# Kernel optimization log

Hardware: AMD Instinct MI355X
Metric: run time of the kernel (lower is better)

Reference implementation:

```python
import jax, jax.numpy as jnp
import numpy as np

# ---------- constants ----------
EPS = 1e-5
_rng = np.random.default_rng(0)
_P = _rng.normal(size=(8, 3))
_P /= np.linalg.norm(_P, axis=1, keepdims=True)

def _y2_np(p):
    x, y, z = p[:, 0], p[:, 1], p[:, 2]
    return np.stack([x * y, y * z, 3 * z * z - 1, x * z, x * x - y * y], axis=-1)

_A2 = np.linalg.pinv(_y2_np(_P)).astype(np.float32)  # [5,8]
P_C = jnp.asarray(_P.astype(np.float32))
A2_C = jnp.asarray(_A2)
NORM_CONST = np.float32(1.0 / np.sqrt(20.0))  # avg_num_neighbors ** -0.5
# res update (buffer zeros, not learnable): sigmoid(0)=0.5
_U = 0.5
C_OLD = np.float32(1.0 / np.sqrt(_U * _U + 1.0))
C_NEW = np.float32(_U * C_OLD)


def _y2(p):  # real l=2 monomial basis on unit vectors
    x, y, z = p[..., 0], p[..., 1], p[..., 2]
    return jnp.stack([x * y, y * z, 3.0 * z * z - 1.0, x * z, x * x - y * y], axis=-1)


def _frame(v):  # [E,3] -> R [E,3,3] with R @ v_hat = z
    n = v / jnp.linalg.norm(v, axis=-1, keepdims=True)
    z = jnp.array([0.0, 0.0, 1.0], v.dtype)
    xa = jnp.array([1.0, 0.0, 0.0], v.dtype)
    a = jnp.where(jnp.abs(n[:, 2:3]) < 0.99, z, xa)
    e1 = jnp.cross(a, n)
    e1 = e1 / jnp.linalg.norm(e1, axis=-1, keepdims=True)
    e2 = jnp.cross(n, e1)
    return jnp.stack([e1, e2, n], axis=1)


def _wigner_d2(R):  # [E,3,3] -> D2 [E,5,5] via sample-point fit
    pts = jnp.einsum('pj,eij->epi', P_C, R)  # R @ p_k, [E,8,3]
    M = _y2(pts)  # [E,8,5] = Y_P @ D^T
    Dt = jnp.einsum('ap,epb->eab', A2_C, M)  # [E,5,5]
    return jnp.swapaxes(Dt, 1, 2)


def _sln(x, w0, b0, w1, w2):  # separable equivariant layernorm, 32x0e+16x1e+8x2e
    s = x[:, :32]
    v1 = x[:, 32:80].reshape(-1, 16, 3)
    v2 = x[:, 80:120].reshape(-1, 8, 5)
    mu = jnp.mean(s, axis=-1, keepdims=True)
    var = jnp.mean((s - mu) ** 2, axis=-1, keepdims=True)
    s = (s - mu) * jax.lax.rsqrt(var + EPS) * w0 + b0
    var1 = jnp.mean(v1 ** 2, axis=(1, 2))  # degree-balanced component variance
    var2 = jnp.mean(v2 ** 2, axis=(1, 2))
    inv = jax.lax.rsqrt(0.5 * (var1 + var2) + EPS)[:, None, None]
    v1 = v1 * inv * w1[None, :, None]
    v2 = v2 * inv * w2[None, :, None]
    return jnp.concatenate([s, v1.reshape(-1, 48), v2.reshape(-1, 40)], axis=-1)


def _ir_linear(x, W0, b0, W1, W2):  # irreps-wise linear 32x0e+16x1e+8x2e -> same
    s = x[:, :32] @ (W0 / np.sqrt(32.0)) + b0
    v1 = jnp.einsum('eui,uv->evi', x[:, 32:80].reshape(-1, 16, 3), W1) / np.sqrt(16.0)
    v2 = jnp.einsum('eui,uv->evi', x[:, 80:120].reshape(-1, 8, 5), W2) / np.sqrt(8.0)
    return jnp.concatenate([s, v1.reshape(-1, 48), v2.reshape(-1, 40)], axis=-1)


def _so2(x_cat, R, D2f, D2b, w):  # SO2 linear with per-edge dynamic weights
    E = x_cat.shape[0]
    w0 = w[:, :8960].reshape(E, 112, 80)
    w1r = w[:, 8960:10112].reshape(E, 48, 24)
    w1i = w[:, 10112:11264].reshape(E, 48, 24)
    w2r = w[:, 11264:11392].reshape(E, 16, 8)
    w2i = w[:, 11392:11520].reshape(E, 16, 8)
    # split concatenated [in + hidden] blocks
    s = jnp.concatenate([x_cat[:, :32], x_cat[:, 120:152]], axis=-1)  # [E,64]
    v1 = jnp.concatenate([x_cat[:, 32:80].reshape(E, 16, 3),
                          x_cat[:, 152:200].reshape(E, 16, 3)], axis=1)  # [E,32,3]
    v2 = jnp.concatenate([x_cat[:, 80:120].reshape(E, 8, 5),
                          x_cat[:, 200:240].reshape(E, 16 // 2, 5)], axis=1)  # [E,16,5]
    # rotate into edge-aligned frame
    v1 = jnp.einsum('eij,euj->eui', R, v1)
    v2 = jnp.einsum('eij,euj->eui', D2f, v2)
    in0 = jnp.concatenate([s, v1[:, :, 1], v2[:, :, 2]], axis=-1)   # m=0, [E,112]
    inn1 = jnp.concatenate([v1[:, :, 0], v2[:, :, 1]], axis=-1)     # m=-1, [E,48]
    inp1 = jnp.concatenate([v1[:, :, 2], v2[:, :, 3]], axis=-1)     # m=+1
    inn2 = v2[:, :, 0]  # m=-2
    inp2 = v2[:, :, 4]  # m=+2
    out0 = jnp.einsum('ei,eio->eo', in0, w0) / np.sqrt(112.0)
    op1 = (jnp.einsum('ei,eio->eo', inp1, w1r) - jnp.einsum('ei,eio->eo', inn1, w1i)) / np.sqrt(48.0)
    on1 = (jnp.einsum('ei,eio->eo', inn1, w1r) + jnp.einsum('ei,eio->eo', inp1, w1i)) / np.sqrt(48.0)
    op2 = (jnp.einsum('ei,eio->eo', inp2, w2r) - jnp.einsum('ei,eio->eo', inn2, w2i)) / np.sqrt(16.0)
    on2 = (jnp.einsum('ei,eio->eo', inn2, w2r) + jnp.einsum('ei,eio->eo', inp2, w2i)) / np.sqrt(16.0)
    s_out = out0[:, :56]
    y1 = jnp.stack([on1[:, :16], out0[:, 56:72], op1[:, :16]], axis=-1)  # [E,16,3]
    y2o = jnp.stack([on2, on1[:, 16:24], out0[:, 72:80], op1[:, 16:24], op2], axis=-1)  # [E,8,5]
    # rotate back
    y1 = jnp.einsum('eij,euj->eui', jnp.swapaxes(R, 1, 2), y1)
    y2o = jnp.einsum('eij,euj->eui', D2b, y2o)
    return jnp.concatenate([s_out, y1.reshape(E, 48), y2o.reshape(E, 40)], axis=-1)  # [E,144]


def _gate(m):  # 32x0e scalars | 24x0e gates | 16x1e+8x2e gated
    s = jax.nn.silu(m[:, :32])
    g = jax.nn.sigmoid(m[:, 32:56])
    v1 = m[:, 56:104].reshape(-1, 16, 3) * g[:, :16, None]
    v2 = m[:, 104:144].reshape(-1, 8, 5) * g[:, 16:24, None]
    return jnp.concatenate([s, v1.reshape(-1, 48), v2.reshape(-1, 40)], axis=-1)


def _env(m, we):  # E3ElementLinear: per-mul elementwise weights
    s = m[:, :32] * we[:, :32]
    v1 = m[:, 32:80].reshape(-1, 16, 3) * we[:, 32:48, None]
    v2 = m[:, 80:120].reshape(-1, 8, 5) * we[:, 48:56, None]
    return jnp.concatenate([s, v1.reshape(-1, 48), v2.reshape(-1, 40)], axis=-1)


def setup_inputs() -> dict:
    key = jax.random.key(0)
    ks = jax.random.split(key, 16)
    N, E, L = 512, 10240, 128
    inp = {
        'latents': jax.random.normal(ks[0], (E, L), jnp.float32),
        'node_features': jax.random.normal(ks[1], (N, 120), jnp.float32),
        'hidden_features': jax.random.normal(ks[2], (E, 120), jnp.float32),
        'node_onehot': jnp.ones((N, 16), jnp.float32),
        'edge_vector': jax.random.normal(ks[3], (E, 3), jnp.float32),
        'W_tp': jax.random.normal(ks[4], (L, 11520), jnp.float32),
        'W_env': jax.random.normal(ks[5], (L, 56), jnp.float32),
        'sln_w0': jnp.ones((32,), jnp.float32),
        'sln_b0': jnp.zeros((32,), jnp.float32),
        'sln_w1': jnp.ones((16,), jnp.float32),
        'sln_w2': jnp.ones((8,), jnp.float32),
        'Wp0': jax.random.normal(ks[6], (32, 32), jnp.float32),
        'bp0': jnp.zeros((32,), jnp.float32),
        'Wp1': jax.random.normal(ks[7], (16, 16), jnp.float32),
        'Wp2': jax.random.normal(ks[8], (8, 8), jnp.float32),
        'Wr0': jax.random.normal(ks[9], (32, 32), jnp.float32),
        'br0': jnp.zeros((32,), jnp.float32),
        'Wr1': jax.random.normal(ks[10], (16, 16), jnp.float32),
        'Wr2': jax.random.normal(ks[11], (8, 8), jnp.float32),
        'atom_type': jax.random.randint(ks[12], (N,), 0, 10, jnp.int32),
        'edge_index': jax.random.randint(ks[13], (2, E), 0, N, jnp.int32),
        'active_edges': jnp.arange(E, dtype=jnp.int32),
    }
    return inp


def reference(latents, node_features, hidden_features, node_onehot, edge_vector,
              W_tp, W_env, sln_w0, sln_b0, sln_w1, sln_w2,
              Wp0, bp0, Wp1, Wp2, Wr0, br0, Wr1, Wr2,
              atom_type, edge_index, active_edges):
    n_nodes = node_features.shape[0]
    center = edge_index[0][active_edges]
    nf = _sln(node_features, sln_w0, sln_b0, sln_w1, sln_w2)
    x_cat = jnp.concatenate([nf[center], hidden_features], axis=-1)  # [E,240]
    v = edge_vector[active_edges]
    R = _frame(v)
    D2f = _wigner_d2(R)
    D2b = _wigner_d2(jnp.swapaxes(R, 1, 2))
    wdyn = latents @ (W_tp / np.sqrt(128.0))  # per-edge dynamic SO2 weights
    msg = _so2(x_cat, R, D2f, D2b, wdyn)
    msg = _gate(msg)
    msg = _ir_linear(msg, Wp0, bp0, Wp1, Wp2)
    wenv = latents[active_edges] @ (W_env / np.sqrt(128.0))
    weighted = _env(msg, wenv)
    new_nf = jax.ops.segment_sum(weighted, center, num_segments=n_nodes)
    new_nf = new_nf * NORM_CONST
    res = _ir_linear(node_features, Wr0, br0, Wr1, Wr2)
    return C_NEW * new_nf + C_OLD * res
```

## Files before the change

### kernel.cpp

```cpp
#include <hip/hip_runtime.h>
#include <math.h>

#define E_TOT   10240
#define N_NODES 512
#define NCOL    11520

typedef unsigned short ushort_t;
typedef unsigned int   uint_t;
typedef __bf16 bf16x8 __attribute__((ext_vector_type(8)));
typedef float  f32x4  __attribute__((ext_vector_type(4)));

constexpr float EPSF        = 1e-5f;
constexpr float INV_SQRT128 = 0.08838834764831845f;
constexpr float INV_SQRT112 = 0.09449111825230681f;
constexpr float INV_SQRT48  = 0.14433756729740643f;
constexpr float INV_SQRT32  = 0.17677669529663687f;
constexpr float INV_SQRT16  = 0.25f;
constexpr float INV_SQRT8   = 0.35355339059327373f;
constexpr float SC0 = INV_SQRT128 * INV_SQRT112;
constexpr float SC1 = INV_SQRT128 * INV_SQRT48;
constexpr float SC2 = INV_SQRT128 * INV_SQRT16;
constexpr float C_OLD_ = 0.8944271909999159f;
constexpr float C_NEW_ = 0.4472135954999579f;
constexpr float NORMC  = 0.22360679774997896f;

__device__ __forceinline__ float wsum(float v) {
#pragma unroll
  for (int off = 32; off > 0; off >>= 1) v += __shfl_xor(v, off, 64);
  return v;
}

__device__ __forceinline__ ushort_t f2bf(float x) {
  uint_t u = __float_as_uint(x);
  u = (u + 0x7fffu + ((u >> 16) & 1u)) >> 16;
  return (ushort_t)u;
}

__device__ __forceinline__ void wigner5(const float q[9], float D[25]) {
  const float q0x=q[0],q0y=q[1],q0z=q[2];
  const float q1x=q[3],q1y=q[4],q1z=q[5];
  const float q2x=q[6],q2y=q[7],q2z=q[8];
  D[0]  = q0x*q1y + q1x*q0y;
  D[1]  = q0y*q1z + q1y*q0z;
  D[2]  = 0.5f*(q0z*q1z);
  D[3]  = q0x*q1z + q1x*q0z;
  D[4]  = 0.5f*(q0x*q1x - q0y*q1y);
  D[5]  = q1x*q2y + q2x*q1y;
  D[6]  = q1y*q2z + q2y*q1z;
  D[7]  = 0.5f*(q1z*q2z);
  D[8]  = q1x*q2z + q2x*q1z;
  D[9]  = 0.5f*(q1x*q2x - q1y*q2y);
  D[10] = 6.f*q2x*q2y;
  D[11] = 6.f*q2y*q2z;
  D[12] = 0.5f*(3.f*q2z*q2z - 1.f);
  D[13] = 6.f*q2x*q2z;
  D[14] = 1.5f*(q2x*q2x - q2y*q2y);
  D[15] = q0x*q2y + q2x*q0y;
  D[16] = q0y*q2z + q2y*q0z;
  D[17] = 0.5f*(q0z*q2z);
  D[18] = q0x*q2z + q2x*q0z;
  D[19] = 0.5f*(q0x*q2x - q0y*q2y);
  D[20] = 2.f*(q0x*q0y - q1x*q1y);
  D[21] = 2.f*(q0y*q0z - q1y*q1z);
  D[22] = 0.5f*(q0z*q0z - q1z*q1z);
  D[23] = 2.f*(q0x*q0z - q1x*q1z);
  D[24] = 0.5f*((q0x*q0x - q1x*q1x) - (q0y*q0y - q1y*q1y));
}

__global__ void k0_latpack(const float* __restrict__ lat,
                           ushort_t* __restrict__ lath, ushort_t* __restrict__ latl) {
  int idx = blockIdx.x*256 + threadIdx.x;
  if (idx >= E_TOT*128) return;
  float x = lat[idx];
  ushort_t h = f2bf(x);
  float hf = __uint_as_float(((uint_t)h) << 16);
  lath[idx] = h;
  latl[idx] = f2bf(x - hf);
}

__global__ void k_pack(const float* __restrict__ Wtp, ushort_t* __restrict__ Wp) {
  const int nt = blockIdx.x;
  const int t = threadIdx.x;
  const int kc = t >> 6, lane = t & 63;
  const int m = lane & 15, kg = lane >> 4;
  int j, mt;
  if (nt < 560)      { j = nt/7; mt = nt - j*7; }
  else if (nt < 704) { int r = nt-560; int p = r/3; j = 80+p; mt = r - p*3; }
  else               { j = 128 + (nt-704); mt = 0; }
  const int i = mt*16 + m;
  int c; float sc;
  if (j < 80)       { c = i*80 + j;               sc = SC0; }
  else if (j < 104) { c = 8960  + i*24 + (j-80);  sc = SC1; }
  else if (j < 128) { c = 10112 + i*24 + (j-104); sc = SC1; }
  else if (j < 136) { c = 11264 + i*8  + (j-128); sc = SC2; }
  else              { c = 11392 + i*8  + (j-136); sc = SC2; }
  ushort_t hi[8], lo[8];
#pragma unroll
  for (int jj = 0; jj < 8; ++jj) {
    int l = kc*32 + kg*8 + jj;
    float w = Wtp[(size_t)l*NCOL + c] * sc;
    ushort_t h = f2bf(w);
    float hf = __uint_as_float(((uint_t)h) << 16);
    hi[jj] = h;
    lo[jj] = f2bf(w - hf);
  }
  size_t base = ((size_t)nt*8 + kc*2)*512 + (size_t)lane*8;
#pragma unroll
  for (int jj = 0; jj < 8; ++jj) {
    Wp[base + jj]       = hi[jj];
    Wp[base + 512 + jj] = lo[jj];
  }
}

__global__ void k1_sln(const float* __restrict__ x_all,
                       const float* __restrict__ w0, const float* __restrict__ b0,
                       const float* __restrict__ w1, const float* __restrict__ w2,
                       float* __restrict__ nf) {
  const int n = blockIdx.x;
  const int t = threadIdx.x;
  const float* x = x_all + n*120;
  float xs = (t < 32) ? x[t] : 0.f;
  float ssum = wsum(xs);
  float ssq  = wsum(xs*xs);
  float mu   = ssum * (1.f/32.f);
  float var  = ssq * (1.f/32.f) - mu*mu;
  float istd = rsqrtf(var + EPSF);
  float q1 = (t < 48) ? x[32+t] : 0.f;
  float v1s = wsum(q1*q1);
  float q2 = (t < 40) ? x[80+t] : 0.f;
  float v2s = wsum(q2*q2);
  float inv = rsqrtf(0.5f*(v1s*(1.f/48.f) + v2s*(1.f/40.f)) + EPSF);
  for (int j = t; j < 120; j += 64) {
    float val = x[j], r;
    if (j < 32)      r = (val - mu)*istd*w0[j] + b0[j];
    else if (j < 80) r = val*inv*w1[(j-32)/3];
    else             r = val*inv*w2[(j-80)/5];
    nf[n*120 + j] = r;
  }
}

__global__ void k2_edge_prep(const float* __restrict__ hid,
                             const float* __restrict__ evec,
                             const int*   __restrict__ eidx,
                             const int*   __restrict__ act,
                             const float* __restrict__ nf,
                             float* __restrict__ invec,
                             float* __restrict__ Rm,
                             float* __restrict__ D2bm) {
  const int e = blockIdx.x*blockDim.x + threadIdx.x;
  if (e >= E_TOT) return;
  const int ae  = act[e];
  const int ctr = eidx[ae];
  float vx = evec[ae*3+0], vy = evec[ae*3+1], vz = evec[ae*3+2];
  float rn = rsqrtf(vx*vx + vy*vy + vz*vz);
  float nx = vx*rn, ny = vy*rn, nz = vz*rn;
  float e1x, e1y, e1z;
  if (fabsf(nz) < 0.99f) { e1x = -ny; e1y = nx;  e1z = 0.f; }
  else                   { e1x = 0.f; e1y = -nz; e1z = ny;  }
  float rl = rsqrtf(e1x*e1x + e1y*e1y + e1z*e1z);
  e1x *= rl; e1y *= rl; e1z *= rl;
  float e2x = ny*e1z - nz*e1y;
  float e2y = nz*e1x - nx*e1z;
  float e2z = nx*e1y - ny*e1x;
  float R[9] = {e1x,e1y,e1z, e2x,e2y,e2z, nx,ny,nz};
#pragma unroll
  for (int j = 0; j < 9; ++j) Rm[e*9 + j] = R[j];
  float Df[25];
  wigner5(R, Df);
  float Rt[9] = {R[0],R[3],R[6], R[1],R[4],R[7], R[2],R[5],R[8]};
  float Db[25];
  wigner5(Rt, Db);
#pragma unroll
  for (int j = 0; j < 25; ++j) D2bm[e*25 + j] = Db[j];
  const float* xa = nf  + (size_t)ctr*120;
  const float* xb = hid + (size_t)e*120;
  float* iv = invec + (size_t)e*240;
#pragma unroll
  for (int j = 0; j < 32; ++j) { iv[j] = xa[j]; iv[32+j] = xb[j]; }
#pragma unroll
  for (int u = 0; u < 32; ++u) {
    const float* src = (u < 16) ? (xa + 32 + 3*u) : (xb + 32 + 3*(u-16));
    float px = src[0], py = src[1], pz = src[2];
    float rx = R[0]*px + R[1]*py + R[2]*pz;
    float ry = R[3]*px + R[4]*py + R[5]*pz;
    float rz = R[6]*px + R[7]*py + R[8]*pz;
    iv[64+u]  = ry;
    iv[112+u] = rx;
    iv[160+u] = rz;
  }
#pragma unroll
  for (int u = 0; u < 16; ++u) {
    const float* src = (u < 8) ? (xa + 80 + 5*u) : (xb + 80 + 5*(u-8));
    float p0 = src[0], p1 = src[1], p2 = src[2], p3 = src[3], p4 = src[4];
    float d[5];
#pragma unroll
    for (int i = 0; i < 5; ++i)
      d[i] = Df[i*5+0]*p0 + Df[i*5+1]*p1 + Df[i*5+2]*p2 + Df[i*5+3]*p3 + Df[i*5+4]*p4;
    iv[96+u]  = d[2];
    iv[144+u] = d[1];
    iv[192+u] = d[3];
    iv[208+u] = d[0];
    iv[224+u] = d[4];
  }
}

__global__ void k2_wenv(const float* __restrict__ lat, const float* __restrict__ Wenv,
                        const int* __restrict__ act, float* __restrict__ wenvo) {
  const int e = blockIdx.x*4 + (threadIdx.x >> 6);
  const int o = threadIdx.x & 63;
  if (o >= 56) return;
  const int ae = act[e];
  const float* lrow = lat + (size_t)ae*128;
  float s = 0.f;
  for (int l = 0; l < 128; ++l) s += lrow[l]*Wenv[l*56 + o];
  wenvo[(size_t)e*56 + o] = s * INV_SQRT128;
}

__global__ __launch_bounds__(256, 3)
void k3_gemm(const ushort_t* __restrict__ Wp,
             const ushort_t* __restrict__ lath,
             const ushort_t* __restrict__ latl,
             const float*  __restrict__ invg,
             float* __restrict__ oa_g) {
  __shared__ float in_lds[32*244];
  const int t = threadIdx.x;
  const int eb = blockIdx.x;
  for (int i = t; i < 32*240; i += 256) {
    int e = i/240, r = i - e*240;
    in_lds[e*244 + r] = invg[(size_t)(eb*32 + e)*240 + r];
  }
  const int wave = t >> 6, lane = t & 63;
  const int le = lane & 15, g = lane >> 4;
  bf16x8 Bh[4][2], Bl[4][2];
  {
    const int e0 = eb*32 + le;
    const int ko = g*8;
#pragma unroll
    for (int kc = 0; kc < 4; ++kc) {
#pragma unroll
      for (int n = 0; n < 2; ++n) {
        size_t off = (size_t)(e0 + 16*n)*128 + kc*32 + ko;
        Bh[kc][n] = *(const bf16x8*)(lath + off);
        Bl[kc][n] = *(const bf16x8*)(latl + off);
      }
    }
  }
  __syncthreads();
  int nt = (blockIdx.y*4 + wave)*90;
  const int ntEnd = nt + 90;
  const int i0b = g*4;
  while (nt < ntEnd) {
    int j, jb, T;
    if (nt < 560)      { j = nt/7;  jb = j*7;  T = 7; }
    else if (nt < 704) { int r = nt - 560; int p = r/3; j = 80 + p; jb = 560 + p*3; T = 3; }
    else               { j = 128 + (nt - 704); jb = nt; T = 1; }
    int mt = nt - jb;
    int cnt = T - mt; { int rem = ntEnd - nt; if (cnt > rem) cnt = rem; }
    int ibA, ibB = 0, slotA, slotB = 0, two;
    float sA = 1.f;
    if (j < 80)       { two = 0; ibA = 0;   slotA = j; }
    else if (j < 104) { two = 1; int o = j-80;  ibA = 160; slotA = 80+o;            ibB = 112; slotB = 104+o; }
    else if (j < 128) { two = 1; int o = j-104; ibA = 112; slotA = 80+o; sA = -1.f; ibB = 160; slotB = 104+o; }
    else if (j < 136) { two = 1; int o = j-128; ibA = 224; slotA = 128+o;           ibB = 208; slotB = 136+o; }
    else              { two = 1; int o = j-136; ibA = 208; slotA = 128+o; sA = -1.f; ibB = 224; slotB = 136+o; }
    float aA0=0.f, aA1=0.f, aB0=0.f, aB1=0.f;
    for (int s = 0; s < cnt; ++s, ++nt, ++mt) {
      const bf16x8* ap = (const bf16x8*)Wp + (size_t)nt*512 + lane;
      f32x4 d0 = {0.f,0.f,0.f,0.f}, d1 = {0.f,0.f,0.f,0.f};
#pragma unroll
      for (int kc = 0; kc < 4; ++kc) {
        bf16x8 Ah = ap[(kc*2+0)*64];
        bf16x8 Al = ap[(kc*2+1)*64];
        d0 = __builtin_amdgcn_mfma_f32_16x16x32_bf16(Ah, Bh[kc][0], d0, 0, 0, 0);
        d1 = __builtin_amdgcn_mfma_f32_16x16x32_bf16(Ah, Bh[kc][1], d1, 0, 0, 0);
        d0 = __builtin_amdgcn_mfma_f32_16x16x32_bf16(Ah, Bl[kc][0], d0, 0, 0, 0);
        d1 = __builtin_amdgcn_mfma_f32_16x16x32_bf16(Ah, Bl[kc][1], d1, 0, 0, 0);
        d0 = __builtin_amdgcn_mfma_f32_16x16x32_bf16(Al, Bh[kc][0], d0, 0, 0, 0);
        d1 = __builtin_amdgcn_mfma_f32_16x16x32_bf16(Al, Bh[kc][1], d1, 0, 0, 0);
      }
      const int i0 = mt*16 + i0b;
      f32x4 iA0 = *(const f32x4*)&in_lds[le*244 + ibA + i0];
      f32x4 iA1 = *(const f32x4*)&in_lds[(le+16)*244 + ibA + i0];
      aA0 += d0[0]*iA0[0] + d0[1]*iA0[1] + d0[2]*iA0[2] + d0[3]*iA0[3];
      aA1 += d1[0]*iA1[0] + d1[1]*iA1[1] + d1[2]*iA1[2] + d1[3]*iA1[3];
      if (two) {
        f32x4 iB0 = *(const f32x4*)&in_lds[le*244 + ibB + i0];
        f32x4 iB1 = *(const f32x4*)&in_lds[(le+16)*244 + ibB + i0];
        aB0 += d0[0]*iB0[0] + d0[1]*iB0[1] + d0[2]*iB0[2] + d0[3]*iB0[3];
        aB1 += d1[0]*iB1[0] + d1[1]*iB1[1] + d1[2]*iB1[2] + d1[3]*iB1[3];
      }
    }
    aA0 += __shfl_xor(aA0, 16, 64); aA0 += __shfl_xor(aA0, 32, 64);
    aA1 += __shfl_xor(aA1, 16, 64); aA1 += __shfl_xor(aA1, 32, 64);
    if (two) {
      aB0 += __shfl_xor(aB0, 16, 64); aB0 += __shfl_xor(aB0, 32, 64);
      aB1 += __shfl_xor(aB1, 16, 64); aB1 += __shfl_xor(aB1, 32, 64);
    }
    if (lane < 16)      atomicAdd(&oa_g[(size_t)(eb*32 + le)*144 + slotA], sA*aA0);
    else if (lane < 32) atomicAdd(&oa_g[(size_t)(eb*32 + 16 + le)*144 + slotA], sA*aA1);
    else if (lane < 48) { if (two) atomicAdd(&oa_g[(size_t)(eb*32 + le)*144 + slotB], aB0); }
    else                { if (two) atomicAdd(&oa_g[(size_t)(eb*32 + 16 + le)*144 + slotB], aB1); }
  }
}

__global__ __launch_bounds__(256)
void k4_epi(const float* __restrict__ oa_g, const float* __restrict__ Rm,
            const float* __restrict__ D2bm, const float* __restrict__ wenvg,
            const int* __restrict__ eidx, const int* __restrict__ act,
            const float* __restrict__ Wp0, const float* __restrict__ bp0,
            const float* __restrict__ Wp1, const float* __restrict__ Wp2,
            float* __restrict__ accg) {
  __shared__ float sc[4][160];
  const int wave = threadIdx.x >> 6, lane = threadIdx.x & 63;
  const int eg = blockIdx.x*4 + wave;
  const float* o_ = oa_g + (size_t)eg*144;
  if (lane < 56) {
    float v = o_[lane];
    sc[wave][lane] = (lane < 32) ? v/(1.f + expf(-v)) : 1.f/(1.f + expf(-v));
  }
  __syncthreads();
  const float* Rr = Rm + (size_t)eg*9;
  const float* Db = D2bm + (size_t)eg*25;
  if (lane < 48) {
    int u = lane/3, cc = lane - u*3;
    float yx = o_[104+u], yy = o_[56+u], yz = o_[80+u];
    float p = Rr[cc]*yx + Rr[3+cc]*yy + Rr[6+cc]*yz;
    sc[wave][56+lane] = p * sc[wave][32+u];
  }
  if (lane >= 48 && lane < 56) {
  }
  __syncthreads();
  if (lane < 40) {
    int u = lane/5, ii = lane - u*5;
    float y0 = o_[136+u], y1v = o_[120+u], y2v = o_[72+u], y3 = o_[96+u], y4 = o_[128+u];
    float p = Db[ii*5+0]*y0 + Db[ii*5+1]*y1v + Db[ii*5+2]*y2v + Db[ii*5+3]*y3 + Db[ii*5+4]*y4;
    sc[wave][104+lane] = p * sc[wave][48+u];
  }
  __syncthreads();
  const float* we = wenvg + (size_t)eg*56;
  const int ctr = eidx[act[eg]];
  float* dst = accg + (size_t)ctr*120;
#pragma unroll
  for (int rnd = 0; rnd < 2; ++rnd) {
    int jo = rnd*64 + lane;
    if (jo < 120) {
      float val;
      if (jo < 32) {
        float s = 0.f;
#pragma unroll
        for (int i2 = 0; i2 < 32; ++i2) s += sc[wave][i2]*Wp0[i2*32 + jo];
        val = (s*INV_SQRT32 + bp0[jo]) * we[jo];
      } else if (jo < 80) {
        int jj = jo-32, v = jj/3, cc = jj - v*3;
        float s = 0.f;
#pragma unroll
        for (int u = 0; u < 16; ++u) s += sc[wave][56 + u*3 + cc]*Wp1[u*16 + v];
        val = s*INV_SQRT16*we[32+v];
      } else {
        int jj = jo-80, v = jj/5, ii = jj - v*5;
        float s = 0.f;
#pragma unroll
        for (int u = 0; u < 8; ++u) s += sc[wave][104 + u*5 + ii]*Wp2[u*8 + v];
        val = s*INV_SQRT8*we[48+v];
      }
      atomicAdd(&dst[jo], val);
    }
  }
}

__global__ void k5_final(const float* __restrict__ x_all,
                         const float* __restrict__ Wr0, const float* __restrict__ br0,
                         const float* __restrict__ Wr1, const float* __restrict__ Wr2,
                         const float* __restrict__ accg,
                         float* __restrict__ out) {
  const int n = blockIdx.x;
  const int t = threadIdx.x;
  if (t >= 120) return;
  const float* x = x_all + n*120;
  float r;
  if (t < 32) {
    float s = 0.f;
#pragma unroll
    for (int i = 0; i < 32; ++i) s += x[i]*Wr0[i*32 + t];
    r = s*INV_SQRT32 + br0[t];
  } else if (t < 80) {
    int j = t - 32, v = j/3, cp = j - 3*v;
    float s = 0.f;
#pragma unroll
    for (int u = 0; u < 16; ++u) s += x[32 + u*3 + cp]*Wr1[u*16 + v];
    r = s*INV_SQRT16;
  } else {
    int j = t - 80, v = j/5, cp = j - 5*v;
    float s = 0.f;
#pragma unroll
    for (int u = 0; u < 8; ++u) s += x[80 + u*5 + cp]*Wr2[u*8 + v];
    r = s*INV_SQRT8;
  }
  out[n*120 + t] = C_NEW_*(NORMC*accg[n*120 + t]) + C_OLD_*r;
}

extern "C" void kernel_launch(void* const* d_in, const int* in_sizes, int n_in,
                              void* d_out, int out_size, void* d_ws, size_t ws_size,
                              hipStream_t stream) {
  const float* lat  = (const float*)d_in[0];
  const float* ndf  = (const float*)d_in[1];
  const float* hid  = (const float*)d_in[2];
  const float* evec = (const float*)d_in[4];
  const float* Wtp  = (const float*)d_in[5];
  const float* Wenv = (const float*)d_in[6];
  const float* w0   = (const float*)d_in[7];
  const float* b0   = (const float*)d_in[8];
  const float* w1   = (const float*)d_in[9];
  const float* w2   = (const float*)d_in[10];
  const float* Wp0  = (const float*)d_in[11];
  const float* bp0  = (const float*)d_in[12];
  const float* Wp1  = (const float*)d_in[13];
  const float* Wp2  = (const float*)d_in[14];
  const float* Wr0  = (const float*)d_in[15];
  const float* br0  = (const float*)d_in[16];
  const float* Wr1  = (const float*)d_in[17];
  const float* Wr2  = (const float*)d_in[18];
  const int*   eidx = (const int*)d_in[20];
  const int*   act  = (const int*)d_in[21];
  float* out = (float*)d_out;

  char* p = (char*)d_ws;
  float*    nf    = (float*)(p);
  float*    invec = (float*)(p + 245760);
  float*    Rm    = (float*)(p + 10076160);
  float*    D2bm  = (float*)(p + 10444800);
  float*    wenv  = (float*)(p + 11468800);
  float*    accg  = (float*)(p + 13762560);
  float*    oa_g  = (float*)(p + 14008320);
  ushort_t* lath  = (ushort_t*)(p + 19906560);
  ushort_t* latl  = (ushort_t*)(p + 22528000);
  ushort_t* Wpack = (ushort_t*)(p + 25149440);

  hipMemsetAsync(accg, 0, 245760, stream);
  hipMemsetAsync(oa_g, 0, 5898240, stream);
  k0_latpack<<<(E_TOT*128 + 255)/256, 256, 0, stream>>>(lat, lath, latl);
  k_pack<<<720, 256, 0, stream>>>(Wtp, Wpack);
  k1_sln<<<N_NODES, 64, 0, stream>>>(ndf, w0, b0, w1, w2, nf);
  k2_edge_prep<<<E_TOT/256, 256, 0, stream>>>(hid, evec, eidx, act, nf, invec, Rm, D2bm);
  k2_wenv<<<E_TOT/4, 256, 0, stream>>>(lat, Wenv, act, wenv);
  k3_gemm<<<dim3(E_TOT/32, 2), 256, 0, stream>>>(Wpack, lath, latl, invec, oa_g);
  k4_epi<<<E_TOT/4, 256, 0, stream>>>(oa_g, Rm, D2bm, wenv, eidx, act, Wp0, bp0, Wp1, Wp2, accg);
  k5_final<<<N_NODES, 128, 0, stream>>>(ndf, Wr0, br0, Wr1, Wr2, accg, out);
}
```

Measured before the change: 336.4 us.

## Remap SO2 GEMM tiles so output channels are M and inputs are accumulated per tile

Repacks the dynamic SO2 weight tiles so each 16-row MFMA tile spans 16 output channels for one input multiplicity, rather than 16 input rows for one output. The per-tile input scalar is then broadcast from LDS and accumulated in registers, which removes the cross-lane shuffle reductions. Atomic adds happen once per segment instead of once per output column. The edge-prep kernel now writes inputs transposed (row-major by feature, edge-contiguous) so LDS staging is coalesced. The GEMM grid is doubled along y with 45 tiles per wave, and the occupancy hint rises to 4. In exchange it issues more atomics per lane at segment ends, adds templated segment code, and spreads work over more blocks.

```diff
diff --git a/kernel.cpp b/kernel.cpp
--- a/kernel.cpp
+++ b/kernel.cpp
@@ -83,17 +83,24 @@
   const int t = threadIdx.x;
   const int kc = t >> 6, lane = t & 63;
   const int m = lane & 15, kg = lane >> 4;
-  int j, mt;
-  if (nt < 560)      { j = nt/7; mt = nt - j*7; }
-  else if (nt < 704) { int r = nt-560; int p = r/3; j = 80+p; mt = r - p*3; }
-  else               { j = 128 + (nt-704); mt = 0; }
-  const int i = mt*16 + m;
+  int col, tt;
+  if (nt < 560)      { col = nt/112; tt = nt - col*112; }
+  else if (nt < 608) { col = 5;  tt = nt-560; }
+  else if (nt < 632) { col = 6;  tt = nt-608; }
+  else if (nt < 680) { col = 7;  tt = nt-632; }
+  else if (nt < 704) { col = 8;  tt = nt-680; }
+  else if (nt < 712) { col = 9;  tt = nt-704; }
+  else               { col = 10; tt = nt-712; }
   int c; float sc;
-  if (j < 80)       { c = i*80 + j;               sc = SC0; }
-  else if (j < 104) { c = 8960  + i*24 + (j-80);  sc = SC1; }
-  else if (j < 128) { c = 10112 + i*24 + (j-104); sc = SC1; }
-  else if (j < 136) { c = 11264 + i*8  + (j-128); sc = SC2; }
-  else              { c = 11392 + i*8  + (j-136); sc = SC2; }
+  switch (col) {
+    case 5:  c = 8960  + tt*24 + m;                      sc = SC1; break;
+    case 6:  c = 8960  + (2*tt + (m>>3))*24 + 16 + (m&7); sc = SC1; break;
+    case 7:  c = 10112 + tt*24 + m;                      sc = SC1; break;
+    case 8:  c = 10112 + (2*tt + (m>>3))*24 + 16 + (m&7); sc = SC1; break;
+    case 9:  c = 11264 + (2*tt + (m>>3))*8 + (m&7);      sc = SC2; break;
+    case 10: c = 11392 + (2*tt + (m>>3))*8 + (m&7);      sc = SC2; break;
+    default: c = tt*80 + col*16 + m;                     sc = SC0; break;
+  }
   ushort_t hi[8], lo[8];
 #pragma unroll
   for (int jj = 0; jj < 8; ++jj) {
@@ -144,7 +151,7 @@
                              const int*   __restrict__ eidx,
                              const int*   __restrict__ act,
                              const float* __restrict__ nf,
-                             float* __restrict__ invec,
+                             float* __restrict__ invT,
                              float* __restrict__ Rm,
                              float* __restrict__ D2bm) {
   const int e = blockIdx.x*blockDim.x + threadIdx.x;
@@ -174,9 +181,9 @@
   for (int j = 0; j < 25; ++j) D2bm[e*25 + j] = Db[j];
   const float* xa = nf  + (size_t)ctr*120;
   const float* xb = hid + (size_t)e*120;
-  float* iv = invec + (size_t)e*240;
-#pragma unroll
-  for (int j = 0; j < 32; ++j) { iv[j] = xa[j]; iv[32+j] = xb[j]; }
+#define IVST(r_, v_) invT[(size_t)(r_)*E_TOT + e] = (v_)
+#pragma unroll
+  for (int j = 0; j < 32; ++j) { IVST(j, xa[j]); IVST(32+j, xb[j]); }
 #pragma unroll
   for (int u = 0; u < 32; ++u) {
     const float* src = (u < 16) ? (xa + 32 + 3*u) : (xb + 32 + 3*(u-16));
@@ -184,9 +191,9 @@
     float rx = R[0]*px + R[1]*py + R[2]*pz;
     float ry = R[3]*px + R[4]*py + R[5]*pz;
     float rz = R[6]*px + R[7]*py + R[8]*pz;
-    iv[64+u]  = ry;
-    iv[112+u] = rx;
-    iv[160+u] = rz;
+    IVST(64+u, ry);
+    IVST(112+u, rx);
+    IVST(160+u, rz);
   }
 #pragma unroll
   for (int u = 0; u < 16; ++u) {
@@ -196,12 +203,13 @@
 #pragma unroll
     for (int i = 0; i < 5; ++i)
       d[i] = Df[i*5+0]*p0 + Df[i*5+1]*p1 + Df[i*5+2]*p2 + Df[i*5+3]*p3 + Df[i*5+4]*p4;
-    iv[96+u]  = d[2];
-    iv[144+u] = d[1];
-    iv[192+u] = d[3];
-    iv[208+u] = d[0];
-    iv[224+u] = d[4];
-  }
+    IVST(96+u,  d[2]);
+    IVST(144+u, d[1]);
+    IVST(192+u, d[3]);
+    IVST(208+u, d[0]);
+    IVST(224+u, d[4]);
+  }
+#undef IVST
 }
 
 __global__ void k2_wenv(const float* __restrict__ lat, const float* __restrict__ Wenv,
@@ -216,18 +224,68 @@
   wenvo[(size_t)e*56 + o] = s * INV_SQRT128;
 }
 
-__global__ __launch_bounds__(256, 3)
+template<bool TWO, bool PAIR>
+__device__ __forceinline__ void run_seg(
+    const bf16x8* __restrict__ W8, int f0, int f1, int tstart,
+    int multP, int multN, int slotP, int slotN, float sgnP,
+    const float* __restrict__ in_lds,
+    const bf16x8 (&Bh)[4][2], const bf16x8 (&Bl)[4][2],
+    int lane, int e0, float* __restrict__ oa) {
+  const int le = lane & 15, g = lane >> 4, gh = g >> 1;
+  f32x4 aP0 = {0,0,0,0}, aP1 = {0,0,0,0}, aN0 = {0,0,0,0}, aN1 = {0,0,0,0};
+  for (int f = f0; f < f1; ++f) {
+    const bf16x8* ap = W8 + (size_t)f*512 + lane;
+    f32x4 d0 = {0,0,0,0}, d1 = {0,0,0,0};
+#pragma unroll
+    for (int kc = 0; kc < 4; ++kc) {
+      bf16x8 Ah = ap[(kc*2+0)*64];
+      bf16x8 Al = ap[(kc*2+1)*64];
+      d0 = __builtin_amdgcn_mfma_f32_16x16x32_bf16(Ah, Bh[kc][0], d0, 0, 0, 0);
+      d1 = __builtin_amdgcn_mfma_f32_16x16x32_bf16(Ah, Bh[kc][1], d1, 0, 0, 0);
+      d0 = __builtin_amdgcn_mfma_f32_16x16x32_bf16(Ah, Bl[kc][0], d0, 0, 0, 0);
+      d1 = __builtin_amdgcn_mfma_f32_16x16x32_bf16(Ah, Bl[kc][1], d1, 0, 0, 0);
+      d0 = __builtin_amdgcn_mfma_f32_16x16x32_bf16(Al, Bh[kc][0], d0, 0, 0, 0);
+      d1 = __builtin_amdgcn_mfma_f32_16x16x32_bf16(Al, Bh[kc][1], d1, 0, 0, 0);
+    }
+    int tt = f - tstart;
+    int idx = PAIR ? (2*tt + gh) : tt;
+    float mP0 = in_lds[(multP+idx)*32 + le];
+    float mP1 = in_lds[(multP+idx)*32 + 16 + le];
+#pragma unroll
+    for (int r = 0; r < 4; ++r) { aP0[r] += mP0*d0[r]; aP1[r] += mP1*d1[r]; }
+    if (TWO) {
+      float mN0 = in_lds[(multN+idx)*32 + le];
+      float mN1 = in_lds[(multN+idx)*32 + 16 + le];
+#pragma unroll
+      for (int r = 0; r < 4; ++r) { aN0[r] += mN0*d0[r]; aN1[r] += mN1*d1[r]; }
+    }
+  }
+#pragma unroll
+  for (int r = 0; r < 4; ++r) {
+    int mm = g*4 + r;
+    int sp = slotP + (PAIR ? (mm & 7) : mm);
+    atomicAdd(&oa[(size_t)e0*144 + sp], sgnP*aP0[r]);
+    atomicAdd(&oa[(size_t)(e0+16)*144 + sp], sgnP*aP1[r]);
+    if (TWO) {
+      int sn = slotN + (PAIR ? (mm & 7) : mm);
+      atomicAdd(&oa[(size_t)e0*144 + sn], aN0[r]);
+      atomicAdd(&oa[(size_t)(e0+16)*144 + sn], aN1[r]);
+    }
+  }
+}
+
+__global__ __launch_bounds__(256, 4)
 void k3_gemm(const ushort_t* __restrict__ Wp,
              const ushort_t* __restrict__ lath,
              const ushort_t* __restrict__ latl,
-             const float*  __restrict__ invg,
+             const float*  __restrict__ invT,
              float* __restrict__ oa_g) {
-  __shared__ float in_lds[32*244];
+  __shared__ float in_lds[240*32];
   const int t = threadIdx.x;
   const int eb = blockIdx.x;
-  for (int i = t; i < 32*240; i += 256) {
-    int e = i/240, r = i - e*240;
-    in_lds[e*244 + r] = invg[(size_t)(eb*32 + e)*240 + r];
+  for (int i = t; i < 240*32; i += 256) {
+    int r = i >> 5, e = i & 31;
+    in_lds[i] = invT[(size_t)r*E_TOT + eb*32 + e];
   }
   const int wave = t >> 6, lane = t & 63;
   const int le = lane & 15, g = lane >> 4;
@@ -246,61 +304,36 @@
     }
   }
   __syncthreads();
-  int nt = (blockIdx.y*4 + wave)*90;
-  const int ntEnd = nt + 90;
-  const int i0b = g*4;
-  while (nt < ntEnd) {
-    int j, jb, T;
-    if (nt < 560)      { j = nt/7;  jb = j*7;  T = 7; }
-    else if (nt < 704) { int r = nt - 560; int p = r/3; j = 80 + p; jb = 560 + p*3; T = 3; }
-    else               { j = 128 + (nt - 704); jb = nt; T = 1; }
-    int mt = nt - jb;
-    int cnt = T - mt; { int rem = ntEnd - nt; if (cnt > rem) cnt = rem; }
-    int ibA, ibB = 0, slotA, slotB = 0, two;
-    float sA = 1.f;
-    if (j < 80)       { two = 0; ibA = 0;   slotA = j; }
-    else if (j < 104) { two = 1; int o = j-80;  ibA = 160; slotA = 80+o;            ibB = 112; slotB = 104+o; }
-    else if (j < 128) { two = 1; int o = j-104; ibA = 112; slotA = 80+o; sA = -1.f; ibB = 160; slotB = 104+o; }
-    else if (j < 136) { two = 1; int o = j-128; ibA = 224; slotA = 128+o;           ibB = 208; slotB = 136+o; }
-    else              { two = 1; int o = j-136; ibA = 208; slotA = 128+o; sA = -1.f; ibB = 224; slotB = 136+o; }
-    float aA0=0.f, aA1=0.f, aB0=0.f, aB1=0.f;
-    for (int s = 0; s < cnt; ++s, ++nt, ++mt) {
-      const bf16x8* ap = (const bf16x8*)Wp + (size_t)nt*512 + lane;
-      f32x4 d0 = {0.f,0.f,0.f,0.f}, d1 = {0.f,0.f,0.f,0.f};
-#pragma unroll
-      for (int kc = 0; kc < 4; ++kc) {
-        bf16x8 Ah = ap[(kc*2+0)*64];
-        bf16x8 Al = ap[(kc*2+1)*64];
-        d0 = __builtin_amdgcn_mfma_f32_16x16x32_bf16(Ah, Bh[kc][0], d0, 0, 0, 0);
-        d1 = __builtin_amdgcn_mfma_f32_16x16x32_bf16(Ah, Bh[kc][1], d1, 0, 0, 0);
-        d0 = __builtin_amdgcn_mfma_f32_16x16x32_bf16(Ah, Bl[kc][0], d0, 0, 0, 0);
-        d1 = __builtin_amdgcn_mfma_f32_16x16x32_bf16(Ah, Bl[kc][1], d1, 0, 0, 0);
-        d0 = __builtin_amdgcn_mfma_f32_16x16x32_bf16(Al, Bh[kc][0], d0, 0, 0, 0);
-        d1 = __builtin_amdgcn_mfma_f32_16x16x32_bf16(Al, Bh[kc][1], d1, 0, 0, 0);
-      }
-      const int i0 = mt*16 + i0b;
-      f32x4 iA0 = *(const f32x4*)&in_lds[le*244 + ibA + i0];
-      f32x4 iA1 = *(const f32x4*)&in_lds[(le+16)*244 + ibA + i0];
-      aA0 += d0[0]*iA0[0] + d0[1]*iA0[1] + d0[2]*iA0[2] + d0[3]*iA0[3];
-      aA1 += d1[0]*iA1[0] + d1[1]*iA1[1] + d1[2]*iA1[2] + d1[3]*iA1[3];
-      if (two) {
-        f32x4 iB0 = *(const f32x4*)&in_lds[le*244 + ibB + i0];
-        f32x4 iB1 = *(const f32x4*)&in_lds[(le+16)*244 + ibB + i0];
-        aB0 += d0[0]*iB0[0] + d0[1]*iB0[1] + d0[2]*iB0[2] + d0[3]*iB0[3];
-        aB1 += d1[0]*iB1[0] + d1[1]*iB1[1] + d1[2]*iB1[2] + d1[3]*iB1[3];
-      }
-    }
-    aA0 += __shfl_xor(aA0, 16, 64); aA0 += __shfl_xor(aA0, 32, 64);
-    aA1 += __shfl_xor(aA1, 16, 64); aA1 += __shfl_xor(aA1, 32, 64);
-    if (two) {
-      aB0 += __shfl_xor(aB0, 16, 64); aB0 += __shfl_xor(aB0, 32, 64);
-      aB1 += __shfl_xor(aB1, 16, 64); aB1 += __shfl_xor(aB1, 32, 64);
-    }
-    if (lane < 16)      atomicAdd(&oa_g[(size_t)(eb*32 + le)*144 + slotA], sA*aA0);
-    else if (lane < 32) atomicAdd(&oa_g[(size_t)(eb*32 + 16 + le)*144 + slotA], sA*aA1);
-    else if (lane < 48) { if (two) atomicAdd(&oa_g[(size_t)(eb*32 + le)*144 + slotB], aB0); }
-    else                { if (two) atomicAdd(&oa_g[(size_t)(eb*32 + 16 + le)*144 + slotB], aB1); }
-  }
+  const bf16x8* W8 = (const bf16x8*)Wp;
+  const int e0 = eb*32 + le;
+  const int f0 = (blockIdx.y*4 + wave)*45, f1 = f0 + 45;
+  int lo, hi;
+#pragma unroll
+  for (int col = 0; col < 5; ++col) {
+    int s = col*112, epos = s + 112;
+    lo = f0 > s ? f0 : s; hi = f1 < epos ? f1 : epos;
+    if (lo < hi)
+      run_seg<false,false>(W8, lo, hi, s, 0, 0, col*16, 0, 1.f,
+                           in_lds, Bh, Bl, lane, e0, oa_g);
+  }
+  lo = f0 > 560 ? f0 : 560; hi = f1 < 608 ? f1 : 608;
+  if (lo < hi) run_seg<true,false>(W8, lo, hi, 560, 160, 112, 80, 104, 1.f,
+                                   in_lds, Bh, Bl, lane, e0, oa_g);
+  lo = f0 > 608 ? f0 : 608; hi = f1 < 632 ? f1 : 632;
+  if (lo < hi) run_seg<true,true>(W8, lo, hi, 608, 160, 112, 96, 120, 1.f,
+                                  in_lds, Bh, Bl, lane, e0, oa_g);
+  lo = f0 > 632 ? f0 : 632; hi = f1 < 680 ? f1 : 680;
+  if (lo < hi) run_seg<true,false>(W8, lo, hi, 632, 112, 160, 80, 104, -1.f,
+                                   in_lds, Bh, Bl, lane, e0, oa_g);
+  lo = f0 > 680 ? f0 : 680; hi = f1 < 704 ? f1 : 704;
+  if (lo < hi) run_seg<true,true>(W8, lo, hi, 680, 112, 160, 96, 120, -1.f,
+                                  in_lds, Bh, Bl, lane, e0, oa_g);
+  lo = f0 > 704 ? f0 : 704; hi = f1 < 712 ? f1 : 712;
+  if (lo < hi) run_seg<true,true>(W8, lo, hi, 704, 224, 208, 128, 136, 1.f,
+                                  in_lds, Bh, Bl, lane, e0, oa_g);
+  lo = f0 > 712 ? f0 : 712; hi = f1 < 720 ? f1 : 720;
+  if (lo < hi) run_seg<true,true>(W8, lo, hi, 712, 208, 224, 128, 136, -1.f,
+                                  in_lds, Bh, Bl, lane, e0, oa_g);
 }
 
 __global__ __launch_bounds__(256)
@@ -326,8 +359,6 @@
     float yx = o_[104+u], yy = o_[56+u], yz = o_[80+u];
     float p = Rr[cc]*yx + Rr[3+cc]*yy + Rr[6+cc]*yz;
     sc[wave][56+lane] = p * sc[wave][32+u];
-  }
-  if (lane >= 48 && lane < 56) {
   }
   __syncthreads();
   if (lane < 40) {
@@ -426,7 +457,7 @@
 
   char* p = (char*)d_ws;
   float*    nf    = (float*)(p);
-  float*    invec = (float*)(p + 245760);
+  float*    invT  = (float*)(p + 245760);
   float*    Rm    = (float*)(p + 10076160);
   float*    D2bm  = (float*)(p + 10444800);
   float*    wenv  = (float*)(p + 11468800);
@@ -441,9 +472,9 @@
   k0_latpack<<<(E_TOT*128 + 255)/256, 256, 0, stream>>>(lat, lath, latl);
   k_pack<<<720, 256, 0, stream>>>(Wtp, Wpack);
   k1_sln<<<N_NODES, 64, 0, stream>>>(ndf, w0, b0, w1, w2, nf);
-  k2_edge_prep<<<E_TOT/256, 256, 0, stream>>>(hid, evec, eidx, act, nf, invec, Rm, D2bm);
+  k2_edge_prep<<<E_TOT/256, 256, 0, stream>>>(hid, evec, eidx, act, nf, invT, Rm, D2bm);
   k2_wenv<<<E_TOT/4, 256, 0, stream>>>(lat, Wenv, act, wenv);
-  k3_gemm<<<dim3(E_TOT/32, 2), 256, 0, stream>>>(Wpack, lath, latl, invec, oa_g);
+  k3_gemm<<<dim3(E_TOT/32, 4), 256, 0, stream>>>(Wpack, lath, latl, invT, oa_g);
   k4_epi<<<E_TOT/4, 256, 0, stream>>>(oa_g, Rm, D2bm, wenv, eidx, act, Wp0, bp0, Wp1, Wp2, accg);
   k5_final<<<N_NODES, 128, 0, stream>>>(ndf, Wr0, br0, Wr1, Wr2, accg, out);
 }
```

Result: slower. 344.1 us (+2.3%).
